# Kernel tuning notes

Hardware: AMD Instinct MI355X
Metric: run time of the kernel (lower is better)

## Reference

```python
import jax, jax.numpy as jnp
import numpy as np

# FIR kernel from resample_kernel=(1,3,3,1): outer product, normalized (gain=1)
_FIR_1D = np.array([1.0, 3.0, 3.0, 1.0], dtype=np.float32)
_FIR = np.outer(_FIR_1D, _FIR_1D)
_FIR = _FIR / _FIR.sum()  # 4x4


def setup_inputs() -> dict:
    key = jax.random.key(0)
    k1, k2, k3 = jax.random.split(key, 3)
    x = jax.random.normal(k1, (16, 256, 64, 64), dtype=jnp.float32)
    # fan_avg uniform init (default_init): variance = 1/fan_avg, fan_in=fan_out=256*9
    scale = float(np.sqrt(3.0 / (256 * 9)))
    w = jax.random.uniform(k2, (256, 256, 3, 3), dtype=jnp.float32, minval=-scale, maxval=scale)
    b = jax.random.normal(k3, (256,), dtype=jnp.float32) * 0.01
    return {"x": x, "w": w, "b": b}


def reference(x, w, b):
    # conv_downsample_2d: upfirdn2d(x, k, pad=(2,2)) then conv2d stride 2, then + bias
    B, C, H, W = x.shape
    # upfirdn2d with up=1, down=1 == zero-padded true convolution with k.
    # k is symmetric so flip is a no-op, but keep it for faithfulness.
    fir = jnp.asarray(_FIR[::-1, ::-1])                       # [4,4]
    fir_k = jnp.tile(fir[None, None, :, :], (C, 1, 1, 1))     # [C,1,4,4] depthwise
    x = jax.lax.conv_general_dilated(
        x, fir_k,
        window_strides=(1, 1),
        padding=((2, 2), (2, 2)),                             # (p+1)//2, p//2 with p=4
        feature_group_count=C,
        dimension_numbers=("NCHW", "OIHW", "NCHW"),
    )                                                          # [B,C,H+1,W+1]
    y = jax.lax.conv_general_dilated(
        x, w,
        window_strides=(2, 2),
        padding="VALID",
        dimension_numbers=("NCHW", "OIHW", "NCHW"),
    )                                                          # [B,outC,H//2,W//2]
    return y + b[None, :, None, None]
```

## Files before the change

### kernel.cpp

```cpp
#include <hip/hip_runtime.h>
#include <hip/hip_bf16.h>

typedef __attribute__((ext_vector_type(8))) short bf16x8;
typedef __attribute__((ext_vector_type(4))) float f32x4;
typedef __attribute__((ext_vector_type(8))) unsigned short u16x8;

#define KD 2304
#define OUT_PER_B (256 * 1024)
#define CGPL 67600

static __device__ __forceinline__ ushort f2bf(float f) {
  union { float f; unsigned int i; } v; v.f = f;
  unsigned int x = v.i;
  x += 0x7fffu + ((x >> 16) & 1u);
  return (ushort)(x >> 16);
}

#define GLDS16(gp, lp)                                                         \
  __builtin_amdgcn_global_load_lds(                                            \
      (const __attribute__((address_space(1))) void*)(gp),                     \
      (__attribute__((address_space(3))) void*)(lp), 16, 0, 0)

#define SWZ(g, r) (((g) & 8) | (((g) ^ (r)) & 7))

#define CVTPK(d, lo, hi) \
  asm("v_cvt_pk_bf16_f32 %0, %1, %2" : "=v"(d) : "v"(lo), "v"(hi))

__global__ __launch_bounds__(256) void k_fir5(const float* __restrict__ x,
                                              ushort* __restrict__ xft,
                                              const float* __restrict__ wsrc,
                                              ushort* __restrict__ wb) {
  __shared__ ushort stageAll[4][8 * 80];
  const int band = blockIdx.x;
  const int cg = blockIdx.y;
  const int b = blockIdx.z;
  const int t = threadIdx.x;
  const int wid = t >> 6, lane = t & 63;
  const int c = lane >> 3, o = lane & 7;
  const int cw = cg * 32 + wid * 8;
  const int h0 = band * 16;
  const int nrows = (band == 4) ? 1 : 16;
  ushort* stage = stageAll[wid];
  const size_t obase = (size_t)(cg * 16 + b) * 4225;

  {
    int flat = band + 5 * (cg + 8 * b);
    for (int iw = flat * 256 + t; iw < 589824; iw += 163840) {
      float v = wsrc[iw];
      int j = iw % 9;
      int t2 = iw / 9;
      wb[(t2 >> 8) * KD + j * 256 + (t2 & 255)] = f2bf(v);
    }
  }

  const float* xrow = x + ((size_t)(b * 256 + cw + c) << 12) + o * 8;

  float4 rA[8], rB[8];
#define LOADR(s, r)                                                            \
  {                                                                            \
    if ((unsigned)(r) < 64u) {                                                 \
      rA[s] = *(const float4*)(xrow + (r) * 64);                               \
      rB[s] = *(const float4*)(xrow + (r) * 64 + 4);                           \
    } else {                                                                   \
      rA[s] = make_float4(0.f, 0.f, 0.f, 0.f);                                 \
      rB[s] = make_float4(0.f, 0.f, 0.f, 0.f);                                 \
    }                                                                          \
  }

  LOADR(6, h0 - 2)
  LOADR(7, h0 - 1)
  LOADR(0, h0)
  LOADR(1, h0 + 1)
  LOADR(2, h0 + 2)

#pragma unroll
  for (int hh = 0; hh < 16; ++hh) {
    if (hh < nrows) {
      const int h = h0 + hh;
      LOADR((hh + 3) & 7, h + 3)

      const int sm2 = (hh + 6) & 7, sm1 = (hh + 7) & 7;
      const int s00 = hh & 7, sp1 = (hh + 1) & 7;
      float v0 = (rA[sm2].x + rA[sp1].x) + 3.f * (rA[sm1].x + rA[s00].x);
      float v1 = (rA[sm2].y + rA[sp1].y) + 3.f * (rA[sm1].y + rA[s00].y);
      float v2 = (rA[sm2].z + rA[sp1].z) + 3.f * (rA[sm1].z + rA[s00].z);
      float v3 = (rA[sm2].w + rA[sp1].w) + 3.f * (rA[sm1].w + rA[s00].w);
      float v4 = (rB[sm2].x + rB[sp1].x) + 3.f * (rB[sm1].x + rB[s00].x);
      float v5 = (rB[sm2].y + rB[sp1].y) + 3.f * (rB[sm1].y + rB[s00].y);
      float v6 = (rB[sm2].z + rB[sp1].z) + 3.f * (rB[sm1].z + rB[s00].z);
      float v7 = (rB[sm2].w + rB[sp1].w) + 3.f * (rB[sm1].w + rB[s00].w);

      float vm1 = __shfl_up(v7, 1);
      float vm2 = __shfl_up(v6, 1);
      float vp  = __shfl_down(v0, 1);
      if (o == 0) { vm1 = 0.f; vm2 = 0.f; }
      if (o == 7) vp = 0.f;

      const float S = 0.015625f;
      float g0 = ((vm2 + v1) + 3.f * (vm1 + v0)) * S;
      float g1 = ((vm1 + v2) + 3.f * (v0 + v1)) * S;
      float g2 = ((v0 + v3) + 3.f * (v1 + v2)) * S;
      float g3 = ((v1 + v4) + 3.f * (v2 + v3)) * S;
      float g4 = ((v2 + v5) + 3.f * (v3 + v4)) * S;
      float g5 = ((v3 + v6) + 3.f * (v4 + v5)) * S;
      float g6 = ((v4 + v7) + 3.f * (v5 + v6)) * S;
      float g7 = ((v5 + vp) + 3.f * (v6 + v7)) * S;

      unsigned d0, d1, d2, d3;
      CVTPK(d0, g0, g1);
      CVTPK(d1, g2, g3);
      CVTPK(d2, g4, g5);
      CVTPK(d3, g6, g7);
      *(uint4*)&stage[c * 80 + ((o ^ c) << 3)] = make_uint4(d0, d1, d2, d3);
      if (o == 7)
        stage[c * 80 + 64] = f2bf((v6 + 3.f * v7) * S);
      __builtin_amdgcn_wave_barrier();

      u16x8 pk;
#pragma unroll
      for (int cc = 0; cc < 8; ++cc)
        pk[cc] = stage[cc * 80 + (((lane >> 3) ^ cc) << 3) + (lane & 7)];
      *(u16x8*)&xft[((obase + h * 65 + lane) << 5) + wid * 8] = pk;
      if (lane == 0) {
        u16x8 p2;
#pragma unroll
        for (int cc = 0; cc < 8; ++cc) p2[cc] = stage[cc * 80 + 64];
        *(u16x8*)&xft[((obase + h * 65 + 64) << 5) + wid * 8] = p2;
      }
      __builtin_amdgcn_wave_barrier();
    }
  }
}

__global__ __launch_bounds__(256) void k_gemm3(const ushort* __restrict__ Wb,
                                               const ushort* __restrict__ Xt,
                                               const float* __restrict__ bias,
                                               float* __restrict__ out) {
  __shared__ ushort lA[128 * 128];
  __shared__ ushort lB[64 * 128];
  const int bid = blockIdx.x;
  const int work = (bid & 7) * 64 + (bid >> 3);
  const int ntile = work >> 1;
  const int mtile = work & 1;
  const int m0 = mtile * 128;
  const int n0 = ntile * 64;
  const int t = threadIdx.x;
  const int wid = t >> 6, lane = t & 63;
  const int wm = wid >> 1, wn = wid & 1;
  const int lrow = lane & 15, kgrp = lane >> 4;

  const ushort* aB[8];
#pragma unroll
  for (int i = 0; i < 8; ++i) {
    int idx = i * 256 + t;
    int row = idx >> 4, gL = idx & 15;
    aB[i] = Wb + (size_t)(m0 + row) * KD + SWZ(gL, row) * 8;
  }
  const ushort* bB[4];
#pragma unroll
  for (int i = 0; i < 4; ++i) {
    int idx = i * 256 + t;
    int row = idx >> 4, gL = idx & 15;
    int sg = SWZ(gL, row);
    int n = n0 + row;
    int b = n >> 10, oh = (n >> 5) & 31, ow = n & 31;
    bB[i] = Xt +
            (((size_t)((sg >> 2) * 16 + b) * 4225 + (2 * oh) * 65 + 2 * ow) << 5) +
            (sg & 3) * 8;
  }

  f32x4 acc[4][2];
#pragma unroll
  for (int i = 0; i < 4; ++i)
#pragma unroll
    for (int j = 0; j < 2; ++j) acc[i][j] = (f32x4){0.f, 0.f, 0.f, 0.f};

  for (int kt = 0; kt < 18; ++kt) {
    const int j = kt >> 1;
    const int dh = j / 3, dw = j - 3 * dh;
    const int boff = (dh * 65 + dw) * 32 + (kt & 1) * (4 * CGPL * 32);
    const int k0 = kt << 7;
    __syncthreads();
#pragma unroll
    for (int i = 0; i < 8; ++i)
      GLDS16(aB[i] + k0, &lA[(i * 256 + t) * 8]);
#pragma unroll
    for (int i = 0; i < 4; ++i)
      GLDS16(bB[i] + boff, &lB[(i * 256 + t) * 8]);
    __syncthreads();

#pragma unroll
    for (int s = 0; s < 4; ++s) {
      bf16x8 Af[4], Bf[2];
#pragma unroll
      for (int f = 0; f < 4; ++f) {
        int row = wm * 64 + f * 16 + lrow;
        Af[f] = *(const bf16x8*)&lA[row * 128 + SWZ(s * 4 + kgrp, row) * 8];
      }
#pragma unroll
      for (int f = 0; f < 2; ++f) {
        int row = wn * 32 + f * 16 + lrow;
        Bf[f] = *(const bf16x8*)&lB[row * 128 + SWZ(s * 4 + kgrp, row) * 8];
      }
#pragma unroll
      for (int fm = 0; fm < 4; ++fm)
#pragma unroll
        for (int fn = 0; fn < 2; ++fn)
          acc[fm][fn] = __builtin_amdgcn_mfma_f32_16x16x32_bf16(
              Af[fm], Bf[fn], acc[fm][fn], 0, 0, 0);
    }
  }

  f32x4 bv[4];
#pragma unroll
  for (int fm = 0; fm < 4; ++fm)
    bv[fm] = *(const f32x4*)(bias + m0 + wm * 64 + fm * 16 + kgrp * 4);

#pragma unroll
  for (int fm = 0; fm < 4; ++fm) {
#pragma unroll
    for (int fn = 0; fn < 2; ++fn) {
      int nn = n0 + wn * 32 + fn * 16 + lrow;
      int oc = m0 + wm * 64 + fm * 16 + kgrp * 4;
      float* op = out + (size_t)(nn >> 10) * OUT_PER_B + (nn & 1023) +
                  (size_t)oc * 1024;
      op[0]    = acc[fm][fn][0] + bv[fm][0];
      op[1024] = acc[fm][fn][1] + bv[fm][1];
      op[2048] = acc[fm][fn][2] + bv[fm][2];
      op[3072] = acc[fm][fn][3] + bv[fm][3];
    }
  }
}

extern "C" void kernel_launch(void* const* d_in, const int* in_sizes, int n_in,
                              void* d_out, int out_size, void* d_ws, size_t ws_size,
                              hipStream_t stream) {
  const float* x    = (const float*)d_in[0];
  const float* w    = (const float*)d_in[1];
  const float* bias = (const float*)d_in[2];
  float* out = (float*)d_out;

  char* ws = (char*)d_ws;
  ushort* xft = (ushort*)ws;
  ushort* wb  = (ushort*)(ws + 34611200);

  k_fir5<<<dim3(5, 8, 16), 256, 0, stream>>>(x, xft, w, wb);
  k_gemm3<<<512, 256, 0, stream>>>(wb, xft, bias, out);
}
```

Before: 60.10 us.

## Double-buffer FIR LDS staging and halve row bands for more FIR blocks

```diff
diff --git a/kernel.cpp b/kernel.cpp
--- a/kernel.cpp
+++ b/kernel.cpp
@@ -30,7 +30,7 @@
                                               ushort* __restrict__ xft,
                                               const float* __restrict__ wsrc,
                                               ushort* __restrict__ wb) {
-  __shared__ ushort stageAll[4][8 * 80];
+  __shared__ ushort stageAll[4][2][8 * 80];
   const int band = blockIdx.x;
   const int cg = blockIdx.y;
   const int b = blockIdx.z;
@@ -38,14 +38,15 @@
   const int wid = t >> 6, lane = t & 63;
   const int c = lane >> 3, o = lane & 7;
   const int cw = cg * 32 + wid * 8;
-  const int h0 = band * 16;
-  const int nrows = (band == 4) ? 1 : 16;
-  ushort* stage = stageAll[wid];
+  const int h0 = band * 8;
+  const int nrows = (band == 8) ? 1 : 8;
+  ushort* stg0 = stageAll[wid][0];
+  ushort* stg1 = stageAll[wid][1];
   const size_t obase = (size_t)(cg * 16 + b) * 4225;
 
   {
-    int flat = band + 5 * (cg + 8 * b);
-    for (int iw = flat * 256 + t; iw < 589824; iw += 163840) {
+    int flat = band + 9 * (cg + 8 * b);
+    for (int iw = flat * 256 + t; iw < 589824; iw += 294912) {
       float v = wsrc[iw];
       int j = iw % 9;
       int t2 = iw / 9;
@@ -67,6 +68,20 @@
     }                                                                          \
   }
 
+#define EMIT(stg, hrow)                                                        \
+  {                                                                            \
+    u16x8 pk;                                                                  \
+    _Pragma("unroll") for (int cc = 0; cc < 8; ++cc)                           \
+        pk[cc] = stg[cc * 80 + (((lane >> 3) ^ cc) << 3) + (lane & 7)];        \
+    *(u16x8*)&xft[((obase + (hrow) * 65 + lane) << 5) + wid * 8] = pk;         \
+    if (lane == 0) {                                                           \
+      u16x8 p2;                                                                \
+      _Pragma("unroll") for (int cc = 0; cc < 8; ++cc)                         \
+          p2[cc] = stg[cc * 80 + 64];                                          \
+      *(u16x8*)&xft[((obase + (hrow) * 65 + 64) << 5) + wid * 8] = p2;         \
+    }                                                                          \
+  }
+
   LOADR(6, h0 - 2)
   LOADR(7, h0 - 1)
   LOADR(0, h0)
@@ -74,10 +89,15 @@
   LOADR(2, h0 + 2)
 
 #pragma unroll
-  for (int hh = 0; hh < 16; ++hh) {
+  for (int hh = 0; hh < 8; ++hh) {
     if (hh < nrows) {
       const int h = h0 + hh;
       LOADR((hh + 3) & 7, h + 3)
+
+      if (hh > 0) {
+        ushort* sp = ((hh - 1) & 1) ? stg1 : stg0;
+        EMIT(sp, h - 1)
+      }
 
       const int sm2 = (hh + 6) & 7, sm1 = (hh + 7) & 7;
       const int s00 = hh & 7, sp1 = (hh + 1) & 7;
@@ -111,24 +131,16 @@
       CVTPK(d1, g2, g3);
       CVTPK(d2, g4, g5);
       CVTPK(d3, g6, g7);
-      *(uint4*)&stage[c * 80 + ((o ^ c) << 3)] = make_uint4(d0, d1, d2, d3);
+      ushort* sc = (hh & 1) ? stg1 : stg0;
+      *(uint4*)&sc[c * 80 + ((o ^ c) << 3)] = make_uint4(d0, d1, d2, d3);
       if (o == 7)
-        stage[c * 80 + 64] = f2bf((v6 + 3.f * v7) * S);
+        sc[c * 80 + 64] = f2bf((v6 + 3.f * v7) * S);
       __builtin_amdgcn_wave_barrier();
-
-      u16x8 pk;
-#pragma unroll
-      for (int cc = 0; cc < 8; ++cc)
-        pk[cc] = stage[cc * 80 + (((lane >> 3) ^ cc) << 3) + (lane & 7)];
-      *(u16x8*)&xft[((obase + h * 65 + lane) << 5) + wid * 8] = pk;
-      if (lane == 0) {
-        u16x8 p2;
-#pragma unroll
-        for (int cc = 0; cc < 8; ++cc) p2[cc] = stage[cc * 80 + 64];
-        *(u16x8*)&xft[((obase + h * 65 + 64) << 5) + wid * 8] = p2;
-      }
-      __builtin_amdgcn_wave_barrier();
-    }
+    }
+  }
+  {
+    ushort* sp = ((nrows - 1) & 1) ? stg1 : stg0;
+    EMIT(sp, h0 + nrows - 1)
   }
 }
 
@@ -244,6 +256,6 @@
   ushort* xft = (ushort*)ws;
   ushort* wb  = (ushort*)(ws + 34611200);
 
-  k_fir5<<<dim3(5, 8, 16), 256, 0, stream>>>(x, xft, w, wb);
+  k_fir5<<<dim3(9, 8, 16), 256, 0, stream>>>(x, xft, w, wb);
   k_gemm3<<<512, 256, 0, stream>>>(wb, xft, bias, out);
 }
```

Result: no change. 61.03 us (+1.5%).

## Split FIR into channel-major output plus separate LDS transpose kernel

Applied to the files above, without the earlier changes.

```diff
diff --git a/kernel.cpp b/kernel.cpp
--- a/kernel.cpp
+++ b/kernel.cpp
@@ -8,6 +8,8 @@
 #define KD 2304
 #define OUT_PER_B (256 * 1024)
 #define CGPL 67600
+#define RPL 72
+#define PPL (65 * RPL)
 
 static __device__ __forceinline__ ushort f2bf(float f) {
   union { float f; unsigned int i; } v; v.f = f;
@@ -26,11 +28,10 @@
 #define CVTPK(d, lo, hi) \
   asm("v_cvt_pk_bf16_f32 %0, %1, %2" : "=v"(d) : "v"(lo), "v"(hi))
 
-__global__ __launch_bounds__(256) void k_fir5(const float* __restrict__ x,
-                                              ushort* __restrict__ xft,
+__global__ __launch_bounds__(256) void k_fir6(const float* __restrict__ x,
+                                              ushort* __restrict__ xfn,
                                               const float* __restrict__ wsrc,
                                               ushort* __restrict__ wb) {
-  __shared__ ushort stageAll[4][8 * 80];
   const int band = blockIdx.x;
   const int cg = blockIdx.y;
   const int b = blockIdx.z;
@@ -38,14 +39,12 @@
   const int wid = t >> 6, lane = t & 63;
   const int c = lane >> 3, o = lane & 7;
   const int cw = cg * 32 + wid * 8;
-  const int h0 = band * 16;
-  const int nrows = (band == 4) ? 1 : 16;
-  ushort* stage = stageAll[wid];
-  const size_t obase = (size_t)(cg * 16 + b) * 4225;
+  const int h0 = band * 8;
+  const int nrows = (band == 8) ? 1 : 8;
 
   {
-    int flat = band + 5 * (cg + 8 * b);
-    for (int iw = flat * 256 + t; iw < 589824; iw += 163840) {
+    int flat = band + 9 * (cg + 8 * b);
+    for (int iw = flat * 256 + t; iw < 589824; iw += 294912) {
       float v = wsrc[iw];
       int j = iw % 9;
       int t2 = iw / 9;
@@ -54,6 +53,7 @@
   }
 
   const float* xrow = x + ((size_t)(b * 256 + cw + c) << 12) + o * 8;
+  ushort* orow = xfn + (size_t)(b * 256 + cw + c) * PPL + o * 8;
 
   float4 rA[8], rB[8];
 #define LOADR(s, r)                                                            \
@@ -74,7 +74,7 @@
   LOADR(2, h0 + 2)
 
 #pragma unroll
-  for (int hh = 0; hh < 16; ++hh) {
+  for (int hh = 0; hh < 8; ++hh) {
     if (hh < nrows) {
       const int h = h0 + hh;
       LOADR((hh + 3) & 7, h + 3)
@@ -111,23 +111,45 @@
       CVTPK(d1, g2, g3);
       CVTPK(d2, g4, g5);
       CVTPK(d3, g6, g7);
-      *(uint4*)&stage[c * 80 + ((o ^ c) << 3)] = make_uint4(d0, d1, d2, d3);
+      *(uint4*)&orow[h * RPL] = make_uint4(d0, d1, d2, d3);
       if (o == 7)
-        stage[c * 80 + 64] = f2bf((v6 + 3.f * v7) * S);
-      __builtin_amdgcn_wave_barrier();
-
-      u16x8 pk;
-#pragma unroll
-      for (int cc = 0; cc < 8; ++cc)
-        pk[cc] = stage[cc * 80 + (((lane >> 3) ^ cc) << 3) + (lane & 7)];
-      *(u16x8*)&xft[((obase + h * 65 + lane) << 5) + wid * 8] = pk;
-      if (lane == 0) {
-        u16x8 p2;
-#pragma unroll
-        for (int cc = 0; cc < 8; ++cc) p2[cc] = stage[cc * 80 + 64];
-        *(u16x8*)&xft[((obase + h * 65 + 64) << 5) + wid * 8] = p2;
-      }
-      __builtin_amdgcn_wave_barrier();
+        orow[h * RPL + 8] = f2bf((v6 + 3.f * v7) * S);
+    }
+  }
+}
+
+__global__ __launch_bounds__(256) void k_tr2(const ushort* __restrict__ xfn,
+                                             ushort* __restrict__ xft) {
+  __shared__ ushort ld[72 * 66];
+  const int h = blockIdx.x;
+  const int c0 = blockIdx.y * 64;
+  const int b = blockIdx.z;
+  const int t = threadIdx.x;
+
+#pragma unroll
+  for (int it = 0; it < 3; ++it) {
+    int idx = it * 256 + t;
+    if (idx < 576) {
+      int c = idx / 9, q = idx - c * 9;
+      u16x8 v = *(const u16x8*)(xfn +
+                 (size_t)(b * 256 + c0 + c) * PPL + h * RPL + q * 8);
+#pragma unroll
+      for (int k = 0; k < 8; ++k)
+        ld[(q * 8 + k) * 66 + (c ^ (k << 3))] = v[k];
+    }
+  }
+  __syncthreads();
+
+#pragma unroll
+  for (int it = 0; it < 3; ++it) {
+    int idx = it * 256 + t;
+    if (idx < 520) {
+      int w = idx >> 3, a = idx & 7;
+      int k7 = w & 7;
+      u16x8 v = *(const u16x8*)&ld[w * 66 + ((a ^ k7) << 3)];
+      int cg = (c0 >> 5) + (a >> 2);
+      *(u16x8*)&xft[(((size_t)(cg * 16 + b) * 4225 + h * 65 + w) << 5) +
+                    (a & 3) * 8] = v;
     }
   }
 }
@@ -241,9 +263,11 @@
   float* out = (float*)d_out;
 
   char* ws = (char*)d_ws;
-  ushort* xft = (ushort*)ws;
-  ushort* wb  = (ushort*)(ws + 34611200);
-
-  k_fir5<<<dim3(5, 8, 16), 256, 0, stream>>>(x, xft, w, wb);
+  ushort* xfn = (ushort*)ws;
+  ushort* xft = (ushort*)(ws + 38338560);
+  ushort* wb  = (ushort*)(ws + 38338560 + 34611200);
+
+  k_fir6<<<dim3(9, 8, 16), 256, 0, stream>>>(x, xfn, w, wb);
+  k_tr2<<<dim3(65, 4, 16), 256, 0, stream>>>(xfn, xft);
   k_gemm3<<<512, 256, 0, stream>>>(wb, xft, bias, out);
 }
```

New measurement: 77.34 us. 1.29x slower.
